# Optimization experiments

Hardware: AMD Instinct MI355X
Metric: run time of the kernel (lower is better)

Reference implementation:

```python
import jax, jax.numpy as jnp
import numpy as np

B, N, DIM, H, DH, K = 4, 2048, 512, 6, 64, 16
KEEP_PROB = 0.9  # 1 - dropout_rate
LOG2PI = float(np.log(2.0 * np.pi))
LOG_PRIOR = float(np.log(1.0 / K))


def setup_inputs() -> dict:
    key = jax.random.key(0)
    ks = jax.random.split(key, 7)
    inputs_q = jax.random.normal(ks[0], (B, N, DIM), dtype=jnp.float32)
    # decoder-style causal mask, shape [B, 1, q_len, kv_len]
    causal = jnp.tril(jnp.ones((N, N), dtype=jnp.float32))
    mask = jnp.broadcast_to(causal[None, None], (B, 1, N, N))
    # dropout keep mask broadcast across the query dim: [B, H, 1, kv_len]
    keep = jax.random.bernoulli(ks[1], KEEP_PROB, (B, H, 1, N)).astype(jnp.float32)
    w_qkv = jax.random.normal(ks[2], (DIM, 3 * H * DH), dtype=jnp.float32) * 0.02
    w_out = jax.random.normal(ks[3], (H * DH, DIM), dtype=jnp.float32) * 0.02
    mu_lookup = jax.random.normal(ks[4], (K, DIM), dtype=jnp.float32)
    logvar_lookup = jax.random.normal(ks[5], (K, DIM), dtype=jnp.float32) * 0.1
    return {
        "inputs_q": inputs_q,
        "mask": mask,
        "keep": keep,
        "w_qkv": w_qkv,
        "w_out": w_out,
        "mu_lookup": mu_lookup,
        "logvar_lookup": logvar_lookup,
    }


def reference(inputs_q, mask, keep, w_qkv, w_out, mu_lookup, logvar_lookup):
    # --- MultiHeadDotProductAttention (self-attn path) ---
    qkv = (inputs_q @ w_qkv).reshape(B, N, 3, H, DH)  # [B,N,3,H,DH]
    q, k, v = qkv[:, :, 0], qkv[:, :, 1], qkv[:, :, 2]
    # bias: 0 where mask > 0, -1e10 elsewhere (note: no 1/sqrt(d) scaling, as in source)
    bias = jnp.where(mask > 0, 0.0, -1e10)
    attn_weights = jnp.einsum('bqhd,bkhd->bhqk', q, k) + bias  # [B,H,N,N]
    attn_weights = jax.nn.softmax(attn_weights, axis=-1)
    # broadcast dropout: mask shared across the query dim
    attn_weights = attn_weights * keep / KEEP_PROB
    attn_out = jnp.einsum('bhqk,bkhd->bqhd', attn_weights, v)
    attn_out = attn_out.reshape(B, N, H * DH) @ w_out  # [B,N,DIM]

    # --- GMM posterior approx q(y|x) ~= p(y|z) (approx_qy_x, vectorized over k) ---
    z = attn_out.mean(axis=1)  # pooled latent, [B,DIM]
    diff = z[:, None, :] - mu_lookup[None]  # [B,K,DIM]
    llh = -0.5 * jnp.sum(
        diff * diff / jnp.exp(logvar_lookup)[None] + logvar_lookup[None] + LOG2PI,
        axis=-1,
    )  # [B,K]
    logLogit_qy_x = llh + LOG_PRIOR
    qy_x = jax.nn.softmax(logLogit_qy_x, axis=1)  # [B,K]

    # combine mixture mean back in so both branches are live in one output
    return attn_out + (qy_x @ mu_lookup)[:, None, :]
```

## Files before the change

kernel.cpp:

```cpp
#include <hip/hip_runtime.h>
#include <cstdint>
#include <cstddef>

#define NH 6
#define NSEQ 2048
#define DIMD 512
#define BATCH 4
#define HD 384
#define LOG2PI_F 1.8378770664093453f

typedef __attribute__((ext_vector_type(8))) short short8;
typedef __attribute__((ext_vector_type(8))) unsigned short ushort8;
typedef __attribute__((ext_vector_type(4))) unsigned short ushort4v;
typedef __attribute__((ext_vector_type(4))) float floatx4;

__device__ inline unsigned short f2bf(float f){
  unsigned int u = __float_as_uint(f);
  u += 0x7FFFu + ((u>>16)&1u);
  return (unsigned short)(u>>16);
}

#define GLD16(gp, lp) __builtin_amdgcn_global_load_lds( \
  (const __attribute__((address_space(1))) void*)(gp), \
  (__attribute__((address_space(3))) void*)(lp), 16, 0, 0)

__global__ __launch_bounds__(256) void convert_x(
    const float* __restrict__ xq, unsigned short* __restrict__ xbf)
{
  int i = blockIdx.x*256 + threadIdx.x;
  floatx4 v = *(const floatx4*)(xq + (size_t)i*4);
  ushort4v r;
  #pragma unroll
  for(int j=0;j<4;j++) r[j] = f2bf(v[j]);
  *(ushort4v*)(xbf + (size_t)i*4) = r;
}

__global__ __launch_bounds__(256) void wtrans(
    const float* __restrict__ src, unsigned short* __restrict__ dst, int R, int C)
{
  __shared__ __attribute__((aligned(16))) unsigned short Ls[64*72];
  const int t = threadIdx.x;
  const int r = t>>2, c0 = (t&3)*16;
  const int d0 = blockIdx.y*64, n0 = blockIdx.x*64;
  #pragma unroll
  for (int j=0;j<16;j+=4){
    floatx4 v = *(const floatx4*)(src + (size_t)(d0+r)*C + n0 + c0 + j);
    #pragma unroll
    for(int jj=0;jj<4;jj++) Ls[r*72 + c0+j+jj] = f2bf(v[jj]);
  }
  __syncthreads();
  #pragma unroll
  for (int j=0;j<16;j+=8){
    ushort8 o;
    #pragma unroll
    for(int jj=0;jj<8;jj++) o[jj] = Ls[(c0+j+jj)*72 + r];
    *(ushort8*)(dst + (size_t)(n0+r)*R + d0 + c0 + j) = o;
  }
}

__global__ __launch_bounds__(256) void vtrans(
    const unsigned short* __restrict__ Vo, unsigned short* __restrict__ Vt)
{
  __shared__ __attribute__((aligned(16))) unsigned short Ls[64*72];
  const int t = threadIdx.x;
  const int r = t>>2, c0 = (t&3)*16;
  const int n0 = blockIdx.x*64, bh = blockIdx.y;
  #pragma unroll
  for (int j=0;j<16;j+=8)
    *(ushort8*)(Ls + r*72 + c0 + j) = *(const ushort8*)(Vo + ((size_t)bh*NSEQ + n0 + r)*64 + c0 + j);
  __syncthreads();
  #pragma unroll
  for (int j=0;j<16;j+=8){
    ushort8 o;
    #pragma unroll
    for(int jj=0;jj<8;jj++) o[jj] = Ls[(c0+j+jj)*72 + r];
    *(ushort8*)(Vt + ((size_t)bh*64 + r)*NSEQ + n0 + c0 + j) = o;
  }
}

__global__ __launch_bounds__(256) void gemm_qkv(
    const unsigned short* __restrict__ A,
    const unsigned short* __restrict__ Bt,
    const float* __restrict__ keep,
    unsigned short* __restrict__ Qo, unsigned short* __restrict__ Ko, unsigned short* __restrict__ Vo)
{
  __shared__ __attribute__((aligned(16))) unsigned short Cs[128*132];
  unsigned short* As = Cs;
  unsigned short* Bs = Cs + 128*64;
  const int tid = threadIdx.x;
  const int w = tid>>6, lane = tid&63;
  const int wr = w>>1, wc = w&1;
  const int quad = lane>>4, l16 = lane&15;
  const int tM = blockIdx.x*128, tN = blockIdx.y*128;
  const int r8 = lane>>3, c8 = (lane&7)*8;
  floatx4 acc[4][4];
  floatx4 zed = {0.f,0.f,0.f,0.f};
  #pragma unroll
  for (int i=0;i<4;i++)
    #pragma unroll
    for(int j=0;j<4;j++) acc[i][j] = zed;

  for (int k0=0; k0<512; k0+=64){
    #pragma unroll
    for (int i=0;i<4;i++){
      int row = w*32 + i*8;
      GLD16(A  + (size_t)(tM+row+r8)*512 + k0 + c8, As + row*64);
      GLD16(Bt + (size_t)(tN+row+r8)*512 + k0 + c8, Bs + row*64);
    }
    __syncthreads();
    #pragma unroll
    for (int kk=0; kk<64; kk+=32){
      short8 af[4], bf[4];
      #pragma unroll
      for(int mt=0;mt<4;mt++)
        af[mt] = *(const short8*)(As + (wr*64+mt*16+l16)*64 + kk + quad*8);
      #pragma unroll
      for(int nt=0;nt<4;nt++)
        bf[nt] = *(const short8*)(Bs + (wc*64+nt*16+l16)*64 + kk + quad*8);
      #pragma unroll
      for(int mt=0;mt<4;mt++)
        #pragma unroll
        for(int nt=0;nt<4;nt++)
          acc[mt][nt] = __builtin_amdgcn_mfma_f32_16x16x32_bf16(af[mt], bf[nt], acc[mt][nt], 0,0,0);
    }
    __syncthreads();
  }
  #pragma unroll
  for(int mt=0;mt<4;mt++)
    #pragma unroll
    for(int nt=0;nt<4;nt++)
      #pragma unroll
      for(int r=0;r<4;r++)
        Cs[(wr*64+mt*16+quad*4+r)*132 + wc*64+nt*16+l16] = f2bf(acc[mt][nt][r]);
  __syncthreads();
  const int row = tid>>1, colh = (tid&1)*64;
  const int gcol0 = tN + colh;
  const int t = gcol0/384, rem = gcol0 - t*384, h = rem>>6;
  const int grow = tM + row, b = grow>>11, n = grow & 2047;
  unsigned short* dst = (t==0 ? Qo : (t==1 ? Ko : Vo)) + ((size_t)((b*NH+h)*NSEQ+n))*64;
  bool vzero = false;
  if (t==2) vzero = (keep[(size_t)(b*NH+h)*NSEQ+n] < 0.5f);
  ushort8 zz;
  #pragma unroll
  for(int q2=0;q2<8;q2++) zz[q2]=0;
  #pragma unroll
  for(int j=0;j<8;j++){
    ushort8 v = *(const ushort8*)(Cs + row*132 + colh + j*8);
    *(ushort8*)(dst + j*8) = vzero ? zz : v;
  }
}

__global__ __launch_bounds__(256, 3) void attn_kernel(
    const unsigned short* __restrict__ Qg, const unsigned short* __restrict__ Kg,
    const unsigned short* __restrict__ VtG,
    unsigned short* __restrict__ atp)
{
  __shared__ __attribute__((aligned(16))) char sm[4*32*68*4 + 4*32*4];
  const int tid = threadIdx.x;
  const int w = tid>>6, lane = tid&63;
  unsigned short* Ps = (unsigned short*)sm + w*(32*72);
  float* Oc   = (float*)sm;
  float* accs = (float*)(sm + 4*32*68*4);
  const int quad = lane>>4, l16 = lane&15;
  const int bid = blockIdx.x;
  const int idx = bid>>3;
  const int bh  = (bid&7) + 8*(idx % 3);
  const int c   = 63 - idx/3;
  const int b = bh/NH, h = bh - b*NH;
  const unsigned short* Qb = Qg  + (size_t)bh*NSEQ*64;
  const unsigned short* Kb = Kg  + (size_t)bh*NSEQ*64;
  const unsigned short* Vb = VtG + (size_t)bh*64*NSEQ;
  const int q0 = c*32;
  const int nkt = (c>>1) + 1;

  short8 qf[2][2];
  #pragma unroll
  for(int mt=0;mt<2;mt++)
    #pragma unroll
    for(int kc=0;kc<2;kc++)
      qf[mt][kc] = *(const short8*)(Qb + (size_t)(q0+mt*16+l16)*64 + kc*32 + quad*8);

  short8 onesf;
  #pragma unroll
  for(int j=0;j<8;j++) onesf[j] = (short)0x3F80;

  floatx4 O[2][4];
  floatx4 accl[2];
  floatx4 zed = {0.f,0.f,0.f,0.f};
  #pragma unroll
  for(int mt=0;mt<2;mt++){
    #pragma unroll
    for(int dt=0;dt<4;dt++) O[mt][dt] = zed;
    accl[mt] = zed;
  }

  for (int kt = w; kt < nkt; kt += 4){
    const int kB = kt*64;
    short8 vf[2][4];
    const unsigned short* vp0 = Vb + kB;
    #pragma unroll
    for(int kh=0;kh<2;kh++)
      #pragma unroll
      for(int dt=0;dt<4;dt++)
        vf[kh][dt] = *(const short8*)(vp0 + (size_t)(dt*16+l16)*NSEQ + kh*32 + quad*8);

    floatx4 sacc[2][4];
    floatx4 m12 = {-12.f,-12.f,-12.f,-12.f};
    #pragma unroll
    for(int mt=0;mt<2;mt++)
      #pragma unroll
      for(int nt=0;nt<4;nt++) sacc[mt][nt] = m12;
    const unsigned short* kp0 = Kb + (size_t)kB*64;
    #pragma unroll
    for(int nt=0;nt<4;nt++){
      short8 kf0 = *(const short8*)(kp0 + (size_t)(nt*16+l16)*64 + quad*8);
      short8 kf1 = *(const short8*)(kp0 + (size_t)(nt*16+l16)*64 + 32 + quad*8);
      #pragma unroll
      for(int mt=0;mt<2;mt++){
        sacc[mt][nt] = __builtin_amdgcn_mfma_f32_16x16x32_bf16(qf[mt][0], kf0, sacc[mt][nt], 0,0,0);
        sacc[mt][nt] = __builtin_amdgcn_mfma_f32_16x16x32_bf16(qf[mt][1], kf1, sacc[mt][nt], 0,0,0);
      }
    }

    const bool dia = (kt == nkt-1);
    #pragma unroll
    for(int mt=0;mt<2;mt++){
      #pragma unroll
      for(int nt=0;nt<4;nt++){
        int key = kB + nt*16 + l16;
        #pragma unroll
        for(int r=0;r<4;r++){
          float p = __expf(sacc[mt][nt][r]);
          if (dia) p = (key <= q0 + mt*16 + quad*4 + r) ? p : 0.f;
          Ps[(mt*16+quad*4+r)*72 + nt*16 + l16] = f2bf(p);
        }
      }
    }
    #pragma unroll
    for(int kh=0;kh<2;kh++){
      #pragma unroll
      for(int mt=0;mt<2;mt++){
        short8 pf = *(const short8*)(Ps + (mt*16+l16)*72 + kh*32 + quad*8);
        accl[mt] = __builtin_amdgcn_mfma_f32_16x16x32_bf16(pf, onesf, accl[mt], 0,0,0);
        #pragma unroll
        for(int dt=0;dt<4;dt++)
          O[mt][dt] = __builtin_amdgcn_mfma_f32_16x16x32_bf16(pf, vf[kh][dt], O[mt][dt], 0,0,0);
      }
    }
  }

  __syncthreads();
  {
    float* Ow = Oc + w*(32*68);
    #pragma unroll
    for(int mt=0;mt<2;mt++){
      #pragma unroll
      for(int dt=0;dt<4;dt++)
        #pragma unroll
        for(int r=0;r<4;r++)
          Ow[(mt*16+quad*4+r)*68 + dt*16 + l16] = O[mt][dt][r];
      if (l16 == 0){
        #pragma unroll
        for(int r=0;r<4;r++)
          accs[w*32 + mt*16+quad*4+r] = accl[mt][r];
      }
    }
  }
  __syncthreads();

  const int orow = tid>>3, oc0 = (tid&7)*8;
  float as = accs[0*32+orow] + accs[1*32+orow] + accs[2*32+orow] + accs[3*32+orow];
  float sc2 = (1.0f/0.9f) / as;
  float vsum[8];
  #pragma unroll
  for(int j=0;j<8;j++) vsum[j] = 0.f;
  #pragma unroll
  for(int s=0;s<4;s++){
    const float* p = Oc + s*(32*68) + orow*68 + oc0;
    #pragma unroll
    for(int j=0;j<8;j++) vsum[j] += p[j];
  }
  ushort8 o;
  #pragma unroll
  for(int j=0;j<8;j++) o[j] = f2bf(vsum[j]*sc2);
  unsigned short* dstp = atp + ((size_t)(b*NSEQ + q0 + orow))*HD + h*64 + oc0;
  *(ushort8*)dstp = o;
}

__global__ __launch_bounds__(256) void gemm_proj(
    const unsigned short* __restrict__ A,
    const unsigned short* __restrict__ Bt,
    float* __restrict__ out,
    float* __restrict__ z)
{
  __shared__ __attribute__((aligned(16))) unsigned short As[128*64];
  __shared__ __attribute__((aligned(16))) unsigned short Bs[128*64];
  const int tid = threadIdx.x;
  const int w = tid>>6, lane = tid&63;
  const int wr = w>>1, wc = w&1;
  const int quad = lane>>4, l16 = lane&15;
  const int tM = blockIdx.x*128, tN = blockIdx.y*128;
  const int r8 = lane>>3, c8 = (lane&7)*8;
  floatx4 acc[4][4];
  floatx4 zed = {0.f,0.f,0.f,0.f};
  #pragma unroll
  for (int i=0;i<4;i++)
    #pragma unroll
    for(int j=0;j<4;j++) acc[i][j] = zed;

  for (int k0=0; k0<384; k0+=64){
    #pragma unroll
    for (int i=0;i<4;i++){
      int row = w*32 + i*8;
      GLD16(A  + (size_t)(tM+row+r8)*384 + k0 + c8, As + row*64);
      GLD16(Bt + (size_t)(tN+row+r8)*384 + k0 + c8, Bs + row*64);
    }
    __syncthreads();
    #pragma unroll
    for (int kk=0; kk<64; kk+=32){
      short8 af[4], bf[4];
      #pragma unroll
      for(int mt=0;mt<4;mt++)
        af[mt] = *(const short8*)(As + (wr*64+mt*16+l16)*64 + kk + quad*8);
      #pragma unroll
      for(int nt=0;nt<4;nt++)
        bf[nt] = *(const short8*)(Bs + (wc*64+nt*16+l16)*64 + kk + quad*8);
      #pragma unroll
      for(int mt=0;mt<4;mt++)
        #pragma unroll
        for(int nt=0;nt<4;nt++)
          acc[mt][nt] = __builtin_amdgcn_mfma_f32_16x16x32_bf16(af[mt], bf[nt], acc[mt][nt], 0,0,0);
    }
    __syncthreads();
  }
  #pragma unroll
  for(int mt=0;mt<4;mt++){
    int grow = tM + wr*64 + mt*16 + quad*4;
    #pragma unroll
    for(int nt=0;nt<4;nt++){
      int gcol = tN + wc*64 + nt*16 + l16;
      #pragma unroll
      for(int r=0;r<4;r++)
        out[(size_t)(grow+r)*512 + gcol] = acc[mt][nt][r];
    }
  }
  #pragma unroll
  for(int nt=0;nt<4;nt++){
    float s = 0.f;
    #pragma unroll
    for(int mt=0;mt<4;mt++)
      #pragma unroll
      for(int r=0;r<4;r++) s += acc[mt][nt][r];
    s += __shfl_xor(s, 16, 64);
    s += __shfl_xor(s, 32, 64);
    if (quad == 0){
      int gcol = tN + wc*64 + nt*16 + l16;
      atomicAdd(&z[(tM>>11)*DIMD + gcol], s);
    }
  }
}

__global__ __launch_bounds__(256) void gmm_kernel(
    const float* __restrict__ z, const float* __restrict__ mu,
    const float* __restrict__ lv, float* __restrict__ c)
{
  __shared__ float sh[16];
  __shared__ float qy[16];
  int tid = threadIdx.x;
  int k = tid>>4, li = tid&15;
  int b = blockIdx.x;
  float part = 0.f;
  for(int d=li; d<DIMD; d+=16){
    float zz = z[b*DIMD+d] * (1.0f/2048.0f);
    float m = mu[k*DIMD+d], l = lv[k*DIMD+d];
    float diff = zz - m;
    part += diff*diff*__expf(-l) + l + LOG2PI_F;
  }
  #pragma unroll
  for(int off=8;off>=1;off>>=1) part += __shfl_xor(part, off, 64);
  if (li==0) sh[k] = part;
  __syncthreads();
  if (tid<16){
    float logit = -0.5f*sh[tid];
    float mx = logit;
    #pragma unroll
    for(int off=8;off>=1;off>>=1) mx = fmaxf(mx, __shfl_xor(mx, off, 64));
    float e = __expf(logit-mx);
    float se = e;
    #pragma unroll
    for(int off=8;off>=1;off>>=1) se += __shfl_xor(se, off, 64);
    qy[tid] = e/se;
  }
  __syncthreads();
  for(int d=tid; d<DIMD; d+=256){
    float accv = 0.f;
    #pragma unroll
    for(int kk=0;kk<16;kk++) accv += qy[kk]*mu[kk*DIMD+d];
    c[b*DIMD+d] = accv;
  }
}

__global__ __launch_bounds__(256) void final_add(
    float* __restrict__ out, const float* __restrict__ c)
{
  size_t i = ((size_t)blockIdx.x*256 + threadIdx.x)*4;
  int d = (int)(i & 511);
  int b = (int)(i >> 20);
  floatx4 a = *(const floatx4*)(out + i);
  floatx4 cc = *(const floatx4*)(c + b*DIMD + d);
  *(floatx4*)(out + i) = a + cc;
}

extern "C" void kernel_launch(void* const* d_in, const int* in_sizes, int n_in,
                              void* d_out, int out_size, void* d_ws, size_t ws_size,
                              hipStream_t stream) {
  const float* inputs_q = (const float*)d_in[0];
  const float* keep  = (const float*)d_in[2];
  const float* w_qkv = (const float*)d_in[3];
  const float* w_out = (const float*)d_in[4];
  const float* mu    = (const float*)d_in[5];
  const float* lv    = (const float*)d_in[6];
  float* out = (float*)d_out;
  char* ws = (char*)d_ws;
  size_t off = 0;
  auto alloc = [&](size_t bytes){ void* p = ws + off; off += (bytes + 255) & ~(size_t)255; return p; };
  unsigned short* Qb  = (unsigned short*)alloc((size_t)24*2048*64*2);
  unsigned short* Kb  = (unsigned short*)alloc((size_t)24*2048*64*2);
  unsigned short* Vo  = (unsigned short*)alloc((size_t)24*2048*64*2);
  unsigned short* Vt  = (unsigned short*)alloc((size_t)24*64*2048*2);
  unsigned short* xbf = (unsigned short*)alloc((size_t)8192*512*2);
  unsigned short* wqT = (unsigned short*)alloc((size_t)1152*512*2);
  unsigned short* woT = (unsigned short*)alloc((size_t)512*384*2);
  unsigned short* atp = (unsigned short*)alloc((size_t)8192*384*2);
  float* z  = (float*)alloc((size_t)4*512*4);
  float* c  = (float*)alloc((size_t)4*512*4);

  hipMemsetAsync(z, 0, 4*512*4, stream);
  convert_x<<<4096, 256, 0, stream>>>(inputs_q, xbf);
  wtrans<<<dim3(18,8), 256, 0, stream>>>(w_qkv, wqT, 512, 1152);
  wtrans<<<dim3(8,6),  256, 0, stream>>>(w_out, woT, 384, 512);
  gemm_qkv<<<dim3(64,9), 256, 0, stream>>>(xbf, wqT, keep, Qb, Kb, Vo);
  vtrans<<<dim3(32,24), 256, 0, stream>>>(Vo, Vt);
  attn_kernel<<<1536, 256, 0, stream>>>(Qb, Kb, Vt, atp);
  gemm_proj<<<dim3(64,4), 256, 0, stream>>>(atp, woT, out, z);
  gmm_kernel<<<4, 256, 0, stream>>>(z, mu, lv, c);
  final_add<<<4096, 256, 0, stream>>>(out, c);
}
```

Baseline: 236.5 us.

## Fuse V transpose into QKV GEMM epilogue and fold log2e into Q

The QKV GEMM epilogue now writes V directly in transposed layout with the dropout keep mask applied, which removes the separate vtrans kernel and the intermediate V buffer round-trip. Q is pre-scaled by log2(e) so the attention kernel can use exp2f instead of __expf, and the softmax offset constant is rescaled to match. The attention kernel's launch bound occupancy hint is raised from 3 to 4 blocks. The transposed store reads LDS column-wise, which may cause bank conflicts, and the higher occupancy hint may force register spills.

Measured after the change: 241.7 us. 2.2% more time.

```diff
diff --git a/kernel.cpp b/kernel.cpp
--- a/kernel.cpp
+++ b/kernel.cpp
@@ -8,6 +8,8 @@
 #define BATCH 4
 #define HD 384
 #define LOG2PI_F 1.8378770664093453f
+#define LOG2E_F 1.4426950408889634f
+#define M12L2_F (-17.312340490667562f)
 
 typedef __attribute__((ext_vector_type(8))) short short8;
 typedef __attribute__((ext_vector_type(8))) unsigned short ushort8;
@@ -58,31 +60,12 @@
   }
 }
 
-__global__ __launch_bounds__(256) void vtrans(
-    const unsigned short* __restrict__ Vo, unsigned short* __restrict__ Vt)
-{
-  __shared__ __attribute__((aligned(16))) unsigned short Ls[64*72];
-  const int t = threadIdx.x;
-  const int r = t>>2, c0 = (t&3)*16;
-  const int n0 = blockIdx.x*64, bh = blockIdx.y;
-  #pragma unroll
-  for (int j=0;j<16;j+=8)
-    *(ushort8*)(Ls + r*72 + c0 + j) = *(const ushort8*)(Vo + ((size_t)bh*NSEQ + n0 + r)*64 + c0 + j);
-  __syncthreads();
-  #pragma unroll
-  for (int j=0;j<16;j+=8){
-    ushort8 o;
-    #pragma unroll
-    for(int jj=0;jj<8;jj++) o[jj] = Ls[(c0+j+jj)*72 + r];
-    *(ushort8*)(Vt + ((size_t)bh*64 + r)*NSEQ + n0 + c0 + j) = o;
-  }
-}
-
 __global__ __launch_bounds__(256) void gemm_qkv(
     const unsigned short* __restrict__ A,
     const unsigned short* __restrict__ Bt,
     const float* __restrict__ keep,
-    unsigned short* __restrict__ Qo, unsigned short* __restrict__ Ko, unsigned short* __restrict__ Vo)
+    unsigned short* __restrict__ Qo, unsigned short* __restrict__ Ko,
+    unsigned short* __restrict__ Vt)
 {
   __shared__ __attribute__((aligned(16))) unsigned short Cs[128*132];
   unsigned short* As = Cs;
@@ -128,29 +111,48 @@
   #pragma unroll
   for(int mt=0;mt<4;mt++)
     #pragma unroll
-    for(int nt=0;nt<4;nt++)
+    for(int nt=0;nt<4;nt++){
+      int gcol = tN + wc*64 + nt*16 + l16;
+      float qs = (gcol < 384) ? LOG2E_F : 1.0f;
       #pragma unroll
       for(int r=0;r<4;r++)
-        Cs[(wr*64+mt*16+quad*4+r)*132 + wc*64+nt*16+l16] = f2bf(acc[mt][nt][r]);
-  __syncthreads();
-  const int row = tid>>1, colh = (tid&1)*64;
-  const int gcol0 = tN + colh;
-  const int t = gcol0/384, rem = gcol0 - t*384, h = rem>>6;
-  const int grow = tM + row, b = grow>>11, n = grow & 2047;
-  unsigned short* dst = (t==0 ? Qo : (t==1 ? Ko : Vo)) + ((size_t)((b*NH+h)*NSEQ+n))*64;
-  bool vzero = false;
-  if (t==2) vzero = (keep[(size_t)(b*NH+h)*NSEQ+n] < 0.5f);
-  ushort8 zz;
-  #pragma unroll
-  for(int q2=0;q2<8;q2++) zz[q2]=0;
-  #pragma unroll
-  for(int j=0;j<8;j++){
-    ushort8 v = *(const ushort8*)(Cs + row*132 + colh + j*8);
-    *(ushort8*)(dst + j*8) = vzero ? zz : v;
-  }
-}
-
-__global__ __launch_bounds__(256, 3) void attn_kernel(
+        Cs[(wr*64+mt*16+quad*4+r)*132 + wc*64+nt*16+l16] = f2bf(acc[mt][nt][r]*qs);
+    }
+  __syncthreads();
+  if (blockIdx.y < 6){
+    const int row = tid>>1, colh = (tid&1)*64;
+    const int gcol0 = tN + colh;
+    const int t = gcol0/384, rem = gcol0 - t*384, h = rem>>6;
+    const int grow = tM + row, b = grow>>11, n = grow & 2047;
+    unsigned short* dst = (t==0 ? Qo : Ko) + ((size_t)((b*NH+h)*NSEQ+n))*64;
+    #pragma unroll
+    for(int j=0;j<8;j++)
+      *(ushort8*)(dst + j*8) = *(const ushort8*)(Cs + row*132 + colh + j*8);
+  } else {
+    const int dcol = tid>>1;
+    const int nh   = (tid&1)*64;
+    const int gcol = tN + dcol;
+    const int rem = gcol - 768, h = rem>>6, dh = rem&63;
+    const int b = tM>>11, nb = tM & 2047;
+    const float* kp = keep + (size_t)(b*NH+h)*NSEQ + nb + nh;
+    unsigned short* dst = Vt + ((size_t)((b*NH+h)*64 + dh))*NSEQ + nb + nh;
+    #pragma unroll
+    for (int j8=0;j8<8;j8++){
+      floatx4 k0 = *(const floatx4*)(kp + j8*8);
+      floatx4 k1 = *(const floatx4*)(kp + j8*8 + 4);
+      ushort8 o;
+      #pragma unroll
+      for(int u=0;u<4;u++)
+        o[u]   = (k0[u] < 0.5f) ? (unsigned short)0 : Cs[(nh + j8*8 + u)*132 + dcol];
+      #pragma unroll
+      for(int u=0;u<4;u++)
+        o[4+u] = (k1[u] < 0.5f) ? (unsigned short)0 : Cs[(nh + j8*8 + 4 + u)*132 + dcol];
+      *(ushort8*)(dst + j8*8) = o;
+    }
+  }
+}
+
+__global__ __launch_bounds__(256, 4) void attn_kernel(
     const unsigned short* __restrict__ Qg, const unsigned short* __restrict__ Kg,
     const unsigned short* __restrict__ VtG,
     unsigned short* __restrict__ atp)
@@ -205,7 +207,7 @@
         vf[kh][dt] = *(const short8*)(vp0 + (size_t)(dt*16+l16)*NSEQ + kh*32 + quad*8);
 
     floatx4 sacc[2][4];
-    floatx4 m12 = {-12.f,-12.f,-12.f,-12.f};
+    floatx4 m12 = {M12L2_F, M12L2_F, M12L2_F, M12L2_F};
     #pragma unroll
     for(int mt=0;mt<2;mt++)
       #pragma unroll
@@ -230,7 +232,7 @@
         int key = kB + nt*16 + l16;
         #pragma unroll
         for(int r=0;r<4;r++){
-          float p = __expf(sacc[mt][nt][r]);
+          float p = exp2f(sacc[mt][nt][r]);
           if (dia) p = (key <= q0 + mt*16 + quad*4 + r) ? p : 0.f;
           Ps[(mt*16+quad*4+r)*72 + nt*16 + l16] = f2bf(p);
         }
@@ -426,7 +428,6 @@
   auto alloc = [&](size_t bytes){ void* p = ws + off; off += (bytes + 255) & ~(size_t)255; return p; };
   unsigned short* Qb  = (unsigned short*)alloc((size_t)24*2048*64*2);
   unsigned short* Kb  = (unsigned short*)alloc((size_t)24*2048*64*2);
-  unsigned short* Vo  = (unsigned short*)alloc((size_t)24*2048*64*2);
   unsigned short* Vt  = (unsigned short*)alloc((size_t)24*64*2048*2);
   unsigned short* xbf = (unsigned short*)alloc((size_t)8192*512*2);
   unsigned short* wqT = (unsigned short*)alloc((size_t)1152*512*2);
@@ -439,8 +440,7 @@
   convert_x<<<4096, 256, 0, stream>>>(inputs_q, xbf);
   wtrans<<<dim3(18,8), 256, 0, stream>>>(w_qkv, wqT, 512, 1152);
   wtrans<<<dim3(8,6),  256, 0, stream>>>(w_out, woT, 384, 512);
-  gemm_qkv<<<dim3(64,9), 256, 0, stream>>>(xbf, wqT, keep, Qb, Kb, Vo);
-  vtrans<<<dim3(32,24), 256, 0, stream>>>(Vo, Vt);
+  gemm_qkv<<<dim3(64,9), 256, 0, stream>>>(xbf, wqT, keep, Qb, Kb, Vt);
   attn_kernel<<<1536, 256, 0, stream>>>(Qb, Kb, Vt, atp);
   gemm_proj<<<dim3(64,4), 256, 0, stream>>>(atp, woT, out, z);
   gmm_kernel<<<4, 256, 0, stream>>>(z, mu, lv, c);
```
